# Kernel tuning notes

Hardware: AMD Instinct MI355X
Metric: run time of the kernel (lower is better)

## Reference

```python
import jax, jax.numpy as jnp
import numpy as np

N = 8192      # num_nodes (adj.shape[0])
CIN = 32
COUT = 32     # must equal CIN so wd = x @ wp @ x.T is (N, N)
CS = 4        # Chebyshev order, static operator
CD = 4        # Chebyshev order, dynamic operator


def setup_inputs() -> dict:
    key = jax.random.key(0)
    k1, k2, k3, k4, k5 = jax.random.split(key, 5)
    x = jax.random.normal(k1, (N, CIN), jnp.float32)
    # scale ws so its spectral radius is O(1); keeps the Chebyshev recurrence numerically tame
    ws = jax.random.normal(k2, (N, N), jnp.float32) * np.float32(1.0 / np.sqrt(N))
    # small scale on wp so wd = x wp x^T has O(1) entries
    wp = jax.random.normal(k3, (CIN, COUT), jnp.float32) * np.float32(1e-3)
    ts = jax.random.normal(k4, (CS, CIN, COUT), jnp.float32)
    td = jax.random.normal(k5, (CD, CIN, COUT), jnp.float32)
    return {"x": x, "ws": ws, "wp": wp, "ts": ts, "td": td}


def reference(x, ws, wp, ts, td):
    # Static operator: Chebyshev expansion T0 = I, T1 = ws, Tk = 2 ws T_{k-1} - T_{k-2}.
    # Run the recurrence on the propagated features y_k = T_k(ws) @ x  (N, cin)
    # instead of forming the (N, N) polynomial matrices -- same math, far less traffic.
    y0 = x                      # T0 @ x
    y1 = ws @ x                 # T1 @ x
    out = y0 @ ts[0]            # shared k=0 term (added into both branches, as in the source)
    out_s = out + y1 @ ts[1]
    for k in range(2, CS):
        y0, y1 = y1, 2.0 * (ws @ y1) - y0
        out_s = out_s + y1 @ ts[k]
    # Dynamic operator: data-dependent graph wd = x @ wp @ x.T  (N, N)
    wd = (x @ wp) @ x.T
    z0 = x
    z1 = wd @ x
    out_d = out + z1 @ td[1]
    for k in range(2, CD):
        z0, z1 = z1, 2.0 * (wd @ z1) - z0
        out_d = out_d + z1 @ td[k]
    # act_func is None in this configuration
    return out_s + out_d
```

## Files before the change

### kernel.cpp

```cpp
#include <hip/hip_runtime.h>
#include <hip/hip_bf16.h>


typedef __attribute__((ext_vector_type(8))) short short8;
typedef __attribute__((ext_vector_type(4))) float floatx4;

__device__ inline short f2bf(float f) {
    union { float f; unsigned u; } v; v.f = f;
    unsigned r = v.u + 0x7FFFu + ((v.u >> 16) & 1u);
    return (short)(r >> 16);
}


__global__ void k_xp(const float* __restrict__ x, const float* __restrict__ wp,
                     float* __restrict__ xp) {
    __shared__ float swp[1024];
    int t = threadIdx.x;
    for (int i = t; i < 1024; i += 256) swp[i] = wp[i];
    __syncthreads();
    int g = blockIdx.x * 256 + t;
    int n = g >> 5, c = g & 31;
    const float* xr = x + n * 32;
    float s = 0.f;
#pragma unroll
    for (int a = 0; a < 32; ++a) s += xr[a] * swp[a * 32 + c];
    xp[g] = s;
}

__global__ void k_gram(const float* __restrict__ x, float* __restrict__ G) {
    int t = threadIdx.x;
    int a = t >> 5, b = t & 31;
    int n0 = blockIdx.x * 256;
    float s = 0.f;
    for (int n = n0; n < n0 + 256; ++n) s += x[n * 32 + a] * x[n * 32 + b];
    atomicAdd(&G[t], s);
}

__global__ void k_coef(const float* __restrict__ G_in, const float* __restrict__ wp,
                       const float* __restrict__ ts, const float* __restrict__ td,
                       float* __restrict__ Cx, float* __restrict__ Cxp) {
    __shared__ float G[1024], W[1024], H1[1024], H2[1024];
    __shared__ float swp[1024], td1[1024], td2[1024], td3[1024], ts0[1024];
    int t = threadIdx.x;
    int a = t >> 5, b = t & 31;
    G[t] = G_in[t]; swp[t] = wp[t]; ts0[t] = ts[t];
    td1[t] = td[1024 + t]; td2[t] = td[2048 + t]; td3[t] = td[3072 + t];
    __syncthreads();
    float s = 0.f;
    for (int c = 0; c < 32; ++c) s += G[a * 32 + c] * swp[c * 32 + b];
    W[t] = s; __syncthreads();
    s = 0.f;
    for (int c = 0; c < 32; ++c) s += W[a * 32 + c] * G[c * 32 + b];
    H1[t] = s; __syncthreads();
    s = 0.f;
    for (int c = 0; c < 32; ++c) s += W[a * 32 + c] * H1[c * 32 + b];
    H2[t] = 2.f * s - G[t]; __syncthreads();
    s = 0.f;
    for (int c = 0; c < 32; ++c)
        s += G[a * 32 + c] * td1[c * 32 + b]
           + 2.f * H1[a * 32 + c] * td2[c * 32 + b]
           + (2.f * H2[a * 32 + c] - G[a * 32 + c]) * td3[c * 32 + b];
    Cxp[t] = s;
    Cx[t] = 2.f * ts0[t] - td2[t];
}

__global__ void k_vt(const float* __restrict__ V, unsigned short* __restrict__ Vt) {
    int g = blockIdx.x * 256 + threadIdx.x;
    int c = g >> 13;
    int k = g & 8191;
    Vt[g] = (unsigned short)f2bf(V[k * 32 + c]);
}

__global__ void k_neg(const float* __restrict__ src, float* __restrict__ dst) {
    int g = blockIdx.x * 256 + threadIdx.x;
    dst[g] = -src[g];
}

__global__ __launch_bounds__(256) void k_gemm(const float* __restrict__ A,
                                              const unsigned short* __restrict__ Vt,
                                              float* __restrict__ Y, float alpha) {
    __shared__ float sm[64 * 64];
    const int t = threadIdx.x;
    const int lane = t & 63;
    const int wv = t >> 6;
    const int l15 = lane & 15;
    const int l4 = lane >> 4;
    const int m0 = blockIdx.x * 64;
    const int k0 = blockIdx.y * 1024;

    floatx4 acc0 = {0.f, 0.f, 0.f, 0.f};
    floatx4 acc1 = {0.f, 0.f, 0.f, 0.f};

    for (int kt = 0; kt < 1024; kt += 64) {
        __syncthreads();
#pragma unroll
        for (int i = 0; i < 4; ++i) {
            int r = i * 16 + (t >> 4);
            int j = t & 15;
            int cch = j ^ (r & 15);
            const float* gsrc = A + (size_t)(m0 + r) * 8192 + (k0 + kt) + cch * 4;
            float* ldst = &sm[(i * 16 + wv * 4) * 64];
            __builtin_amdgcn_global_load_lds(
                (const __attribute__((address_space(1))) unsigned int*)gsrc,
                (__attribute__((address_space(3))) unsigned int*)ldst,
                16, 0, 0);
        }
        __syncthreads();
#pragma unroll
        for (int kh = 0; kh < 2; ++kh) {
            int rl = wv * 16 + l15;
            int jb = kh * 8 + l4 * 2;
            floatx4 f0 = *(floatx4*)&sm[rl * 64 + ((jb    ) ^ l15) * 4];
            floatx4 f1 = *(floatx4*)&sm[rl * 64 + ((jb + 1) ^ l15) * 4];
            short8 av;
            av[0] = f2bf(f0.x); av[1] = f2bf(f0.y); av[2] = f2bf(f0.z); av[3] = f2bf(f0.w);
            av[4] = f2bf(f1.x); av[5] = f2bf(f1.y); av[6] = f2bf(f1.z); av[7] = f2bf(f1.w);
            int kk = k0 + kt + kh * 32 + l4 * 8;
            short8 b0 = *(const short8*)(Vt + (size_t)l15 * 8192 + kk);
            short8 b1 = *(const short8*)(Vt + (size_t)(16 + l15) * 8192 + kk);
            acc0 = __builtin_amdgcn_mfma_f32_16x16x32_bf16(av, b0, acc0, 0, 0, 0);
            acc1 = __builtin_amdgcn_mfma_f32_16x16x32_bf16(av, b1, acc1, 0, 0, 0);
        }
    }
    int row0 = m0 + wv * 16 + l4 * 4;
#pragma unroll
    for (int i = 0; i < 4; ++i) {
        atomicAdd(&Y[(size_t)(row0 + i) * 32 + l15], alpha * acc0[i]);
        atomicAdd(&Y[(size_t)(row0 + i) * 32 + 16 + l15], alpha * acc1[i]);
    }
}

__global__ void k_final(const float* __restrict__ x, const float* __restrict__ xp,
                        const float* __restrict__ y1, const float* __restrict__ y2,
                        const float* __restrict__ y3, const float* __restrict__ Cx,
                        const float* __restrict__ Cxp, const float* __restrict__ ts,
                        float* __restrict__ out) {
    __shared__ float m0[1024], m1[1024], m2[1024], m3[1024], m4[1024];
    int t = threadIdx.x;
    for (int i = t; i < 1024; i += 256) {
        m0[i] = Cx[i]; m1[i] = Cxp[i];
        m2[i] = ts[1024 + i]; m3[i] = ts[2048 + i]; m4[i] = ts[3072 + i];
    }
    __syncthreads();
    int g = blockIdx.x * 256 + t;
    int n = g >> 5, c = g & 31;
    const float* xr  = x  + n * 32;
    const float* xpr = xp + n * 32;
    const float* y1r = y1 + n * 32;
    const float* y2r = y2 + n * 32;
    const float* y3r = y3 + n * 32;
    float s = 0.f;
#pragma unroll
    for (int a = 0; a < 32; ++a) {
        s += xr[a]  * m0[a * 32 + c]
           + xpr[a] * m1[a * 32 + c]
           + y1r[a] * m2[a * 32 + c]
           + y2r[a] * m3[a * 32 + c]
           + y3r[a] * m4[a * 32 + c];
    }
    out[g] = s;
}

extern "C" void kernel_launch(void* const* d_in, const int* in_sizes, int n_in,
                              void* d_out, int out_size, void* d_ws, size_t ws_size,
                              hipStream_t stream) {
    const float* x  = (const float*)d_in[0];
    const float* ws = (const float*)d_in[1];
    const float* wp = (const float*)d_in[2];
    const float* ts = (const float*)d_in[3];
    const float* td = (const float*)d_in[4];
    float* out = (float*)d_out;

    float* xp  = (float*)d_ws;
    float* y1  = xp + 262144;
    float* y2  = y1 + 262144;
    float* y3  = y2 + 262144;
    float* G   = y3 + 262144;
    float* Cx  = G + 1024;
    float* Cxp = Cx + 1024;
    unsigned short* Vt = (unsigned short*)(Cxp + 1024);

    hipMemsetAsync(G, 0, 1024 * sizeof(float), stream);
    k_xp<<<1024, 256, 0, stream>>>(x, wp, xp);
    k_gram<<<32, 1024, 0, stream>>>(x, G);
    k_coef<<<1, 1024, 0, stream>>>(G, wp, ts, td, Cx, Cxp);

    dim3 gg(128, 8);
    k_vt<<<1024, 256, 0, stream>>>(x, Vt);
    hipMemsetAsync(y1, 0, 262144 * sizeof(float), stream);
    k_gemm<<<gg, 256, 0, stream>>>(ws, Vt, y1, 1.0f);
    k_vt<<<1024, 256, 0, stream>>>(y1, Vt);
    k_neg<<<1024, 256, 0, stream>>>(x, y2);
    k_gemm<<<gg, 256, 0, stream>>>(ws, Vt, y2, 2.0f);
    k_vt<<<1024, 256, 0, stream>>>(y2, Vt);
    k_neg<<<1024, 256, 0, stream>>>(y1, y3);
    k_gemm<<<gg, 256, 0, stream>>>(ws, Vt, y3, 2.0f);

    k_final<<<1024, 256, 0, stream>>>(x, xp, y1, y2, y3, Cx, Cxp, ts, out);
}
```

Measured before the change: 561.6 us.

## Cache bf16 copy of ws and replace atomics with split-K partial reductions

The first GEMM converts ws to bf16 and writes that copy to workspace, so the second and third GEMMs stream half as many bytes from a bf16 operand. Atomic accumulation is replaced by per-split-K partial buffers that a new kernel reduces, applying the Chebyshev axpy and producing the transposed bf16 operand for the next GEMM. Prep kernels (xp, Gram, transpose) are fused into one, which removes several launches and memsets. The cost is an extra 128MB bf16 write in the first GEMM and more workspace.

Result: no change. 567.3 us (+1.0%).

```diff
diff --git a/kernel.cpp b/kernel.cpp
--- a/kernel.cpp
+++ b/kernel.cpp
@@ -5,45 +5,69 @@
 typedef __attribute__((ext_vector_type(8))) short short8;
 typedef __attribute__((ext_vector_type(4))) float floatx4;
 
-__device__ inline short f2bf(float f) {
+__device__ inline unsigned short f2bf(float f) {
     union { float f; unsigned u; } v; v.f = f;
     unsigned r = v.u + 0x7FFFu + ((v.u >> 16) & 1u);
-    return (short)(r >> 16);
-}
-
-
-__global__ void k_xp(const float* __restrict__ x, const float* __restrict__ wp,
-                     float* __restrict__ xp) {
+    return (unsigned short)(r >> 16);
+}
+
+__global__ __launch_bounds__(256) void k_prep(const float* __restrict__ x,
+                                              const float* __restrict__ wp,
+                                              float* __restrict__ xp,
+                                              float* __restrict__ Gpart,
+                                              unsigned short* __restrict__ Vt) {
+    __shared__ float sx[8192];
     __shared__ float swp[1024];
-    int t = threadIdx.x;
+    __shared__ unsigned short st[32][264];
+    const int t = threadIdx.x;
+    const int n0 = blockIdx.x * 256;
+    const floatx4* x4 = (const floatx4*)(x + (size_t)n0 * 32);
+    floatx4* sx4 = (floatx4*)sx;
+#pragma unroll
+    for (int i = 0; i < 8; ++i) sx4[i * 256 + t] = x4[i * 256 + t];
     for (int i = t; i < 1024; i += 256) swp[i] = wp[i];
     __syncthreads();
-    int g = blockIdx.x * 256 + t;
-    int n = g >> 5, c = g & 31;
-    const float* xr = x + n * 32;
-    float s = 0.f;
-#pragma unroll
-    for (int a = 0; a < 32; ++a) s += xr[a] * swp[a * 32 + c];
-    xp[g] = s;
-}
-
-__global__ void k_gram(const float* __restrict__ x, float* __restrict__ G) {
-    int t = threadIdx.x;
-    int a = t >> 5, b = t & 31;
-    int n0 = blockIdx.x * 256;
-    float s = 0.f;
-    for (int n = n0; n < n0 + 256; ++n) s += x[n * 32 + a] * x[n * 32 + b];
-    atomicAdd(&G[t], s);
-}
-
-__global__ void k_coef(const float* __restrict__ G_in, const float* __restrict__ wp,
+
+    float row[32];
+#pragma unroll
+    for (int a = 0; a < 32; ++a) row[a] = sx[t * 32 + a];
+
+    float* xpr = xp + (size_t)(n0 + t) * 32;
+#pragma unroll
+    for (int c = 0; c < 32; ++c) {
+        float s = 0.f;
+#pragma unroll
+        for (int a = 0; a < 32; ++a) s += row[a] * swp[a * 32 + c];
+        xpr[c] = s;
+        st[c][t] = f2bf(row[c]);
+    }
+
+    const int a = t >> 3;
+    const int b = 4 * (t & 7);
+    float g0 = 0.f, g1 = 0.f, g2 = 0.f, g3 = 0.f;
+    for (int i = 0; i < 256; ++i) {
+        float va = sx[i * 32 + a];
+        floatx4 vb = *(floatx4*)&sx[i * 32 + b];
+        g0 += va * vb.x; g1 += va * vb.y; g2 += va * vb.z; g3 += va * vb.w;
+    }
+    floatx4 g = {g0, g1, g2, g3};
+    *(floatx4*)&Gpart[(size_t)blockIdx.x * 1024 + (size_t)(a * 32 + b)] = g;
+
+    __syncthreads();
+#pragma unroll
+    for (int c = 0; c < 32; ++c) Vt[(size_t)c * 8192 + n0 + t] = st[c][t];
+}
+
+__global__ void k_coef(const float* __restrict__ Gpart, const float* __restrict__ wp,
                        const float* __restrict__ ts, const float* __restrict__ td,
                        float* __restrict__ Cx, float* __restrict__ Cxp) {
     __shared__ float G[1024], W[1024], H1[1024], H2[1024];
     __shared__ float swp[1024], td1[1024], td2[1024], td3[1024], ts0[1024];
     int t = threadIdx.x;
     int a = t >> 5, b = t & 31;
-    G[t] = G_in[t]; swp[t] = wp[t]; ts0[t] = ts[t];
+    float gs = 0.f;
+    for (int p = 0; p < 32; ++p) gs += Gpart[p * 1024 + t];
+    G[t] = gs; swp[t] = wp[t]; ts0[t] = ts[t];
     td1[t] = td[1024 + t]; td2[t] = td[2048 + t]; td3[t] = td[3072 + t];
     __syncthreads();
     float s = 0.f;
@@ -64,22 +88,12 @@
     Cx[t] = 2.f * ts0[t] - td2[t];
 }
 
-__global__ void k_vt(const float* __restrict__ V, unsigned short* __restrict__ Vt) {
-    int g = blockIdx.x * 256 + threadIdx.x;
-    int c = g >> 13;
-    int k = g & 8191;
-    Vt[g] = (unsigned short)f2bf(V[k * 32 + c]);
-}
-
-__global__ void k_neg(const float* __restrict__ src, float* __restrict__ dst) {
-    int g = blockIdx.x * 256 + threadIdx.x;
-    dst[g] = -src[g];
-}
-
-__global__ __launch_bounds__(256) void k_gemm(const float* __restrict__ A,
+template <bool CONV>
+__global__ __launch_bounds__(256) void k_gemm(const float* __restrict__ Af,
+                                              const unsigned short* __restrict__ Ab,
+                                              unsigned short* __restrict__ wsb_out,
                                               const unsigned short* __restrict__ Vt,
-                                              float* __restrict__ Y, float alpha) {
-    __shared__ float sm[64 * 64];
+                                              float* __restrict__ Ypart) {
     const int t = threadIdx.x;
     const int lane = t & 63;
     const int wv = t >> 6;
@@ -91,43 +105,116 @@
     floatx4 acc0 = {0.f, 0.f, 0.f, 0.f};
     floatx4 acc1 = {0.f, 0.f, 0.f, 0.f};
 
-    for (int kt = 0; kt < 1024; kt += 64) {
-        __syncthreads();
-#pragma unroll
-        for (int i = 0; i < 4; ++i) {
-            int r = i * 16 + (t >> 4);
-            int j = t & 15;
-            int cch = j ^ (r & 15);
-            const float* gsrc = A + (size_t)(m0 + r) * 8192 + (k0 + kt) + cch * 4;
-            float* ldst = &sm[(i * 16 + wv * 4) * 64];
-            __builtin_amdgcn_global_load_lds(
-                (const __attribute__((address_space(1))) unsigned int*)gsrc,
-                (__attribute__((address_space(3))) unsigned int*)ldst,
-                16, 0, 0);
+    if (CONV) {
+        __shared__ float sm[64 * 64];
+        for (int kt = 0; kt < 1024; kt += 64) {
+            __syncthreads();
+#pragma unroll
+            for (int i = 0; i < 4; ++i) {
+                int r = i * 16 + (t >> 4);
+                int j = t & 15;
+                int cch = j ^ (r & 15);
+                const float* gsrc = Af + (size_t)(m0 + r) * 8192 + (k0 + kt) + cch * 4;
+                float* ldst = &sm[(i * 16 + wv * 4) * 64];
+                __builtin_amdgcn_global_load_lds(
+                    (const __attribute__((address_space(1))) unsigned int*)gsrc,
+                    (__attribute__((address_space(3))) unsigned int*)ldst, 16, 0, 0);
+            }
+            __syncthreads();
+#pragma unroll
+            for (int kh = 0; kh < 2; ++kh) {
+                int rl = wv * 16 + l15;
+                int jb = kh * 8 + l4 * 2;
+                floatx4 f0 = *(floatx4*)&sm[rl * 64 + ((jb    ) ^ l15) * 4];
+                floatx4 f1 = *(floatx4*)&sm[rl * 64 + ((jb + 1) ^ l15) * 4];
+                short8 av;
+                av[0] = f2bf(f0.x); av[1] = f2bf(f0.y); av[2] = f2bf(f0.z); av[3] = f2bf(f0.w);
+                av[4] = f2bf(f1.x); av[5] = f2bf(f1.y); av[6] = f2bf(f1.z); av[7] = f2bf(f1.w);
+                int kk = k0 + kt + kh * 32 + l4 * 8;
+                *(short8*)(wsb_out + (size_t)(m0 + rl) * 8192 + kk) = av;
+                short8 b0 = *(const short8*)(Vt + (size_t)l15 * 8192 + kk);
+                short8 b1 = *(const short8*)(Vt + (size_t)(16 + l15) * 8192 + kk);
+                acc0 = __builtin_amdgcn_mfma_f32_16x16x32_bf16(av, b0, acc0, 0, 0, 0);
+                acc1 = __builtin_amdgcn_mfma_f32_16x16x32_bf16(av, b1, acc1, 0, 0, 0);
+            }
         }
-        __syncthreads();
-#pragma unroll
-        for (int kh = 0; kh < 2; ++kh) {
-            int rl = wv * 16 + l15;
-            int jb = kh * 8 + l4 * 2;
-            floatx4 f0 = *(floatx4*)&sm[rl * 64 + ((jb    ) ^ l15) * 4];
-            floatx4 f1 = *(floatx4*)&sm[rl * 64 + ((jb + 1) ^ l15) * 4];
-            short8 av;
-            av[0] = f2bf(f0.x); av[1] = f2bf(f0.y); av[2] = f2bf(f0.z); av[3] = f2bf(f0.w);
-            av[4] = f2bf(f1.x); av[5] = f2bf(f1.y); av[6] = f2bf(f1.z); av[7] = f2bf(f1.w);
-            int kk = k0 + kt + kh * 32 + l4 * 8;
-            short8 b0 = *(const short8*)(Vt + (size_t)l15 * 8192 + kk);
-            short8 b1 = *(const short8*)(Vt + (size_t)(16 + l15) * 8192 + kk);
-            acc0 = __builtin_amdgcn_mfma_f32_16x16x32_bf16(av, b0, acc0, 0, 0, 0);
-            acc1 = __builtin_amdgcn_mfma_f32_16x16x32_bf16(av, b1, acc1, 0, 0, 0);
+    } else {
+        __shared__ unsigned short sm16[64 * 64];
+        for (int kt = 0; kt < 1024; kt += 64) {
+            __syncthreads();
+#pragma unroll
+            for (int i = 0; i < 2; ++i) {
+                int r = i * 32 + (t >> 3);
+                int j = t & 7;
+                int cch = j ^ (r & 7);
+                const unsigned short* gsrc =
+                    Ab + (size_t)(m0 + r) * 8192 + (k0 + kt) + cch * 8;
+                unsigned short* ldst = &sm16[(i * 32 + wv * 8) * 64];
+                __builtin_amdgcn_global_load_lds(
+                    (const __attribute__((address_space(1))) unsigned int*)gsrc,
+                    (__attribute__((address_space(3))) unsigned int*)ldst, 16, 0, 0);
+            }
+            __syncthreads();
+#pragma unroll
+            for (int kh = 0; kh < 2; ++kh) {
+                int rl = wv * 16 + l15;
+                short8 av = *(short8*)&sm16[rl * 64 + ((kh * 4 + l4) ^ (rl & 7)) * 8];
+                int kk = k0 + kt + kh * 32 + l4 * 8;
+                short8 b0 = *(const short8*)(Vt + (size_t)l15 * 8192 + kk);
+                short8 b1 = *(const short8*)(Vt + (size_t)(16 + l15) * 8192 + kk);
+                acc0 = __builtin_amdgcn_mfma_f32_16x16x32_bf16(av, b0, acc0, 0, 0, 0);
+                acc1 = __builtin_amdgcn_mfma_f32_16x16x32_bf16(av, b1, acc1, 0, 0, 0);
+            }
         }
     }
+    float* yp = Ypart + (size_t)blockIdx.y * 262144;
     int row0 = m0 + wv * 16 + l4 * 4;
 #pragma unroll
     for (int i = 0; i < 4; ++i) {
-        atomicAdd(&Y[(size_t)(row0 + i) * 32 + l15], alpha * acc0[i]);
-        atomicAdd(&Y[(size_t)(row0 + i) * 32 + 16 + l15], alpha * acc1[i]);
-    }
+        yp[(size_t)(row0 + i) * 32 + l15] = acc0[i];
+        yp[(size_t)(row0 + i) * 32 + 16 + l15] = acc1[i];
+    }
+}
+
+__global__ __launch_bounds__(256) void k_trans(const float* __restrict__ Ypart,
+                                               const float* __restrict__ prev,
+                                               float alpha, float beta,
+                                               float* __restrict__ y,
+                                               unsigned short* __restrict__ Vt) {
+    __shared__ unsigned short st[32][264];
+    const int t = threadIdx.x;
+    const int n0 = blockIdx.x * 256;
+    const size_t base4 = (size_t)n0 * 8;
+    floatx4 r[8];
+#pragma unroll
+    for (int j = 0; j < 8; ++j) r[j] = {0.f, 0.f, 0.f, 0.f};
+    for (int p = 0; p < 8; ++p) {
+        const floatx4* P4 = (const floatx4*)(Ypart + (size_t)p * 262144);
+#pragma unroll
+        for (int j = 0; j < 8; ++j) r[j] += P4[base4 + j * 256 + t];
+    }
+    const floatx4* prev4 = (const floatx4*)prev;
+    floatx4* y4 = (floatx4*)y;
+#pragma unroll
+    for (int j = 0; j < 8; ++j) {
+        floatx4 pv = prev4[base4 + j * 256 + t];
+        floatx4 v;
+        v.x = alpha * r[j].x + beta * pv.x;
+        v.y = alpha * r[j].y + beta * pv.y;
+        v.z = alpha * r[j].z + beta * pv.z;
+        v.w = alpha * r[j].w + beta * pv.w;
+        y4[base4 + j * 256 + t] = v;
+        int q = j * 256 + t;
+        int lr = q >> 3;
+        int c4 = (q & 7) * 4;
+        st[c4 + 0][lr] = f2bf(v.x);
+        st[c4 + 1][lr] = f2bf(v.y);
+        st[c4 + 2][lr] = f2bf(v.z);
+        st[c4 + 3][lr] = f2bf(v.w);
+    }
+    __syncthreads();
+#pragma unroll
+    for (int c = 0; c < 32; ++c) Vt[(size_t)c * 8192 + n0 + t] = st[c][t];
 }
 
 __global__ void k_final(const float* __restrict__ x, const float* __restrict__ xp,
@@ -144,11 +231,11 @@
     __syncthreads();
     int g = blockIdx.x * 256 + t;
     int n = g >> 5, c = g & 31;
-    const float* xr  = x  + n * 32;
-    const float* xpr = xp + n * 32;
-    const float* y1r = y1 + n * 32;
-    const float* y2r = y2 + n * 32;
-    const float* y3r = y3 + n * 32;
+    const float* xr  = x  + (size_t)n * 32;
+    const float* xpr = xp + (size_t)n * 32;
+    const float* y1r = y1 + (size_t)n * 32;
+    const float* y2r = y2 + (size_t)n * 32;
+    const float* y3r = y3 + (size_t)n * 32;
     float s = 0.f;
 #pragma unroll
     for (int a = 0; a < 32; ++a) {
@@ -171,30 +258,27 @@
     const float* td = (const float*)d_in[4];
     float* out = (float*)d_out;
 
-    float* xp  = (float*)d_ws;
+    char* w = (char*)d_ws;
+    unsigned short* wsb = (unsigned short*)w;
+    float* Ppart = (float*)(w + 134217728);
+    float* xp  = Ppart + 2097152;
     float* y1  = xp + 262144;
     float* y2  = y1 + 262144;
     float* y3  = y2 + 262144;
-    float* G   = y3 + 262144;
-    float* Cx  = G + 1024;
+    unsigned short* Vt = (unsigned short*)(y3 + 262144);
+    float* Gpart = (float*)(Vt + 262144);
+    float* Cx  = Gpart + 32768;
     float* Cxp = Cx + 1024;
-    unsigned short* Vt = (unsigned short*)(Cxp + 1024);
-
-    hipMemsetAsync(G, 0, 1024 * sizeof(float), stream);
-    k_xp<<<1024, 256, 0, stream>>>(x, wp, xp);
-    k_gram<<<32, 1024, 0, stream>>>(x, G);
-    k_coef<<<1, 1024, 0, stream>>>(G, wp, ts, td, Cx, Cxp);
 
     dim3 gg(128, 8);
-    k_vt<<<1024, 256, 0, stream>>>(x, Vt);
-    hipMemsetAsync(y1, 0, 262144 * sizeof(float), stream);
-    k_gemm<<<gg, 256, 0, stream>>>(ws, Vt, y1, 1.0f);
-    k_vt<<<1024, 256, 0, stream>>>(y1, Vt);
-    k_neg<<<1024, 256, 0, stream>>>(x, y2);
-    k_gemm<<<gg, 256, 0, stream>>>(ws, Vt, y2, 2.0f);
-    k_vt<<<1024, 256, 0, stream>>>(y2, Vt);
-    k_neg<<<1024, 256, 0, stream>>>(y1, y3);
-    k_gemm<<<gg, 256, 0, stream>>>(ws, Vt, y3, 2.0f);
+    k_prep<<<32, 256, 0, stream>>>(x, wp, xp, Gpart, Vt);
+    k_coef<<<1, 1024, 0, stream>>>(Gpart, wp, ts, td, Cx, Cxp);
+    k_gemm<true><<<gg, 256, 0, stream>>>(ws, nullptr, wsb, Vt, Ppart);
+    k_trans<<<32, 256, 0, stream>>>(Ppart, x, 1.0f, 0.0f, y1, Vt);
+    k_gemm<false><<<gg, 256, 0, stream>>>(nullptr, wsb, nullptr, Vt, Ppart);
+    k_trans<<<32, 256, 0, stream>>>(Ppart, x, 2.0f, -1.0f, y2, Vt);
+    k_gemm<false><<<gg, 256, 0, stream>>>(nullptr, wsb, nullptr, Vt, Ppart);
+    k_trans<<<32, 256, 0, stream>>>(Ppart, y1, 2.0f, -1.0f, y3, Vt);
 
     k_final<<<1024, 256, 0, stream>>>(x, xp, y1, y2, y3, Cx, Cxp, ts, out);
 }
```
